# Performance work log

Measured on AMD Instinct MI355X. Metric: run time of the kernel, lower is better.

The kernel has to match this reference:

```python
import jax, jax.numpy as jnp
import numpy as np

BN_EPS = 1e-3  # keras BatchNormalization default epsilon
D = 128
EDGE_DIM = 16
N_NODES = 50000
N_EDGES = 800000

def setup_inputs() -> dict:
    key = jax.random.key(0)
    ks = jax.random.split(key, 12)
    inp = {
        'node_feat': jax.random.normal(ks[0], (N_NODES, D), jnp.float32),
        'edge_feat': jax.random.normal(ks[1], (N_EDGES, EDGE_DIM), jnp.float32),
        'src': jax.random.randint(ks[2], (N_EDGES,), 0, N_NODES, jnp.int32),
        'dst': jax.random.randint(ks[3], (N_EDGES,), 0, N_NODES, jnp.int32),
        # EdgeEncoder: Dense(2*D) -> Dense(D)
        'We1': jax.random.normal(ks[4], (EDGE_DIM, 2 * D), jnp.float32) * 0.05,
        'be1': jnp.zeros((2 * D,), jnp.float32),
        'We2': jax.random.normal(ks[5], (2 * D, D), jnp.float32) * 0.05,
        'be2': jnp.zeros((D,), jnp.float32),
        # GINNodeUpdate eps (shape (1,) weight)
        'eps': jax.random.normal(ks[6], (1,), jnp.float32) * 0.05,
        # MLP: Dense(2*D) -> BN -> relu -> Dense(D)
        'Wm1': jax.random.normal(ks[7], (D, 2 * D), jnp.float32) * 0.05,
        'bm1': jnp.zeros((2 * D,), jnp.float32),
        'g1': jnp.ones((2 * D,), jnp.float32),
        'b1': jnp.zeros((2 * D,), jnp.float32),
        'm1': jnp.zeros((2 * D,), jnp.float32),
        'v1': jnp.ones((2 * D,), jnp.float32),
        'Wm2': jax.random.normal(ks[8], (2 * D, D), jnp.float32) * 0.05,
        'bm2': jnp.zeros((D,), jnp.float32),
        # outer BN after MLP
        'g2': jnp.ones((D,), jnp.float32),
        'b2': jnp.zeros((D,), jnp.float32),
        'm2': jnp.zeros((D,), jnp.float32),
        'v2': jnp.ones((D,), jnp.float32),
    }
    return inp

def _bn(x, gamma, beta, mean, var):
    return (x - mean) * jax.lax.rsqrt(var + BN_EPS) * gamma + beta

def reference(node_feat, edge_feat, src, dst, We1, be1, We2, be2, eps,
              Wm1, bm1, g1, b1, m1, v1, Wm2, bm2, g2, b2, m2, v2):
    # EdgeEncoder on raw edge features -> [E, D]
    e = (edge_feat @ We1 + be1) @ We2 + be2
    # combine_type='sum' with broadcast-from-sender gather, message_fn=relu
    msg = jax.nn.relu(e + node_feat[src])          # [E, D]
    # pool_to_receiver: segment-sum scatter to target nodes
    pooled = jax.ops.segment_sum(msg, dst, num_segments=node_feat.shape[0])  # [N, D]
    # GINNodeUpdate: MLP((1+eps)*node + pooled) then BN
    h = (1.0 + eps) * node_feat + pooled
    h = jax.nn.relu(_bn(h @ Wm1 + bm1, g1, b1, m1, v1)) @ Wm2 + bm2
    return _bn(h, g2, b2, m2, v2)
```

## Files before the change

kernel.cpp:

```cpp
#include <hip/hip_runtime.h>

#define D 128
#define TWO_D 256
#define EDIM 16
#define BN_EPS 1e-3f
#define NT 16
#define CAP 48

__device__ __forceinline__ float4 fma4(float4 a, float s, float4 w) {
    a.x = fmaf(s, w.x, a.x);
    a.y = fmaf(s, w.y, a.y);
    a.z = fmaf(s, w.z, a.z);
    a.w = fmaf(s, w.w, a.w);
    return a;
}

__device__ __forceinline__ unsigned bf16pk(float a, float b) {
    unsigned ua = __float_as_uint(a); ua = (ua + 0x7FFFu + ((ua >> 16) & 1u)) >> 16;
    unsigned ub = __float_as_uint(b); ub = (ub + 0x7FFFu + ((ub >> 16) & 1u)) & 0xFFFF0000u;
    return ua | ub;
}
__device__ __forceinline__ float bf_lo(unsigned u) { return __uint_as_float(u << 16); }
__device__ __forceinline__ float bf_hi(unsigned u) { return __uint_as_float(u & 0xFFFF0000u); }

__device__ __forceinline__ void mlp_tile(
    int tid, int n0, const float* hbuf, float* tbuf,
    const float* __restrict__ Wm1, const float* __restrict__ bm1,
    const float* __restrict__ g1, const float* __restrict__ b1,
    const float* __restrict__ m1, const float* __restrict__ v1,
    const float* __restrict__ Wm2, const float* __restrict__ bm2,
    const float* __restrict__ g2, const float* __restrict__ b2,
    const float* __restrict__ m2, const float* __restrict__ v2,
    float* __restrict__ out)
{
    {
        const int g = tid >> 7;
        const int c = tid & 127;
        float acc[8][2];
#pragma unroll
        for (int n = 0; n < 8; ++n) { acc[n][0] = 0.f; acc[n][1] = 0.f; }

        for (int k0 = 0; k0 < D; k0 += 4) {
            float wa[4], wb[4];
#pragma unroll
            for (int kk = 0; kk < 4; ++kk) {
                wa[kk] = Wm1[(k0 + kk) * TWO_D + c];
                wb[kk] = Wm1[(k0 + kk) * TWO_D + c + 128];
            }
#pragma unroll
            for (int n = 0; n < 8; ++n) {
                float4 h4 = *(const float4*)&hbuf[(g * 8 + n) * D + k0];
                acc[n][0] = fmaf(h4.x, wa[0], acc[n][0]);
                acc[n][0] = fmaf(h4.y, wa[1], acc[n][0]);
                acc[n][0] = fmaf(h4.z, wa[2], acc[n][0]);
                acc[n][0] = fmaf(h4.w, wa[3], acc[n][0]);
                acc[n][1] = fmaf(h4.x, wb[0], acc[n][1]);
                acc[n][1] = fmaf(h4.y, wb[1], acc[n][1]);
                acc[n][1] = fmaf(h4.z, wb[2], acc[n][1]);
                acc[n][1] = fmaf(h4.w, wb[3], acc[n][1]);
            }
        }
        const float s1a = g1[c] * rsqrtf(v1[c] + BN_EPS);
        const float t1a = (bm1[c] - m1[c]) * s1a + b1[c];
        const int c2 = c + 128;
        const float s1b = g1[c2] * rsqrtf(v1[c2] + BN_EPS);
        const float t1b = (bm1[c2] - m1[c2]) * s1b + b1[c2];
#pragma unroll
        for (int n = 0; n < 8; ++n) {
            tbuf[(g * 8 + n) * TWO_D + c]  = fmaxf(fmaf(acc[n][0], s1a, t1a), 0.f);
            tbuf[(g * 8 + n) * TWO_D + c2] = fmaxf(fmaf(acc[n][1], s1b, t1b), 0.f);
        }
    }
    __syncthreads();

    {
        const int q = tid >> 6;
        const int d = tid & 63;
        float acc2[4][2];
#pragma unroll
        for (int n = 0; n < 4; ++n) { acc2[n][0] = 0.f; acc2[n][1] = 0.f; }

        for (int k0 = 0; k0 < TWO_D; k0 += 4) {
            float wa[4], wb[4];
#pragma unroll
            for (int kk = 0; kk < 4; ++kk) {
                wa[kk] = Wm2[(k0 + kk) * D + d];
                wb[kk] = Wm2[(k0 + kk) * D + d + 64];
            }
#pragma unroll
            for (int n = 0; n < 4; ++n) {
                float4 t4 = *(const float4*)&tbuf[(q * 4 + n) * TWO_D + k0];
                acc2[n][0] = fmaf(t4.x, wa[0], acc2[n][0]);
                acc2[n][0] = fmaf(t4.y, wa[1], acc2[n][0]);
                acc2[n][0] = fmaf(t4.z, wa[2], acc2[n][0]);
                acc2[n][0] = fmaf(t4.w, wa[3], acc2[n][0]);
                acc2[n][1] = fmaf(t4.x, wb[0], acc2[n][1]);
                acc2[n][1] = fmaf(t4.y, wb[1], acc2[n][1]);
                acc2[n][1] = fmaf(t4.z, wb[2], acc2[n][1]);
                acc2[n][1] = fmaf(t4.w, wb[3], acc2[n][1]);
            }
        }
        const float s2a = g2[d] * rsqrtf(v2[d] + BN_EPS);
        const float t2a = (bm2[d] - m2[d]) * s2a + b2[d];
        const int d2 = d + 64;
        const float s2b = g2[d2] * rsqrtf(v2[d2] + BN_EPS);
        const float t2b = (bm2[d2] - m2[d2]) * s2b + b2[d2];
#pragma unroll
        for (int n = 0; n < 4; ++n) {
            size_t row = (size_t)(n0 + q * 4 + n) * D;
            out[row + d]  = fmaf(acc2[n][0], s2a, t2a);
            out[row + d2] = fmaf(acc2[n][1], s2b, t2b);
        }
    }
}

__global__ __launch_bounds__(128)
void fold_and_zero(const float* __restrict__ We1,
                   const float* __restrict__ be1,
                   const float* __restrict__ We2,
                   const float* __restrict__ be2,
                   float* __restrict__ Wf,
                   float* __restrict__ bf,
                   int*   __restrict__ cnt,
                   int n_nodes)
{
    const int b = blockIdx.x;
    if (b <= EDIM) {
        const int k = b, d = threadIdx.x;
        if (k < EDIM) {
            float acc = 0.f;
            for (int j = 0; j < TWO_D; j += 4) {
                acc = fmaf(We1[k * TWO_D + j + 0], We2[(j + 0) * D + d], acc);
                acc = fmaf(We1[k * TWO_D + j + 1], We2[(j + 1) * D + d], acc);
                acc = fmaf(We1[k * TWO_D + j + 2], We2[(j + 2) * D + d], acc);
                acc = fmaf(We1[k * TWO_D + j + 3], We2[(j + 3) * D + d], acc);
            }
            Wf[k * D + d] = acc;
        } else {
            float acc = be2[d];
            for (int j = 0; j < TWO_D; j += 4) {
                acc = fmaf(be1[j + 0], We2[(j + 0) * D + d], acc);
                acc = fmaf(be1[j + 1], We2[(j + 1) * D + d], acc);
                acc = fmaf(be1[j + 2], We2[(j + 2) * D + d], acc);
                acc = fmaf(be1[j + 3], We2[(j + 3) * D + d], acc);
            }
            bf[d] = acc;
        }
    } else {
        int i = (b - (EDIM + 1)) * 128 + threadIdx.x;
        if (i < n_nodes) cnt[i] = 0;
    }
}

__global__ __launch_bounds__(256)
void scatter_ef(const float* __restrict__ edge_feat,
                const int* __restrict__ src, const int* __restrict__ dst,
                int* __restrict__ cnt,
                int* __restrict__ s_src,
                uint4* __restrict__ s_ef,
                int n_edges)
{
    int i = blockIdx.x * blockDim.x + threadIdx.x;
    if (i >= n_edges) return;
    const int d = dst[i];
    const float4* e4 = (const float4*)(edge_feat + (size_t)i * EDIM);
    const float4 f0 = e4[0], f1 = e4[1], f2 = e4[2], f3 = e4[3];
    const int s = src[i];
    const int pos = atomicAdd(&cnt[d], 1);
    if (pos < CAP) {
        const size_t r = (size_t)d * CAP + pos;
        s_src[r] = s;
        s_ef[r * 2 + 0] = make_uint4(bf16pk(f0.x, f0.y), bf16pk(f0.z, f0.w),
                                     bf16pk(f1.x, f1.y), bf16pk(f1.z, f1.w));
        s_ef[r * 2 + 1] = make_uint4(bf16pk(f2.x, f2.y), bf16pk(f2.z, f2.w),
                                     bf16pk(f3.x, f3.y), bf16pk(f3.z, f3.w));
    }
}

__global__ __launch_bounds__(256, 3)
void fused_ef(const uint4* __restrict__ s_ef,
              const int*   __restrict__ s_src,
              const int*   __restrict__ cnt,
              const float* __restrict__ node_feat,
              const float* __restrict__ Wf,
              const float* __restrict__ bf,
              const float* __restrict__ eps,
              const float* __restrict__ Wm1, const float* __restrict__ bm1,
              const float* __restrict__ g1, const float* __restrict__ b1,
              const float* __restrict__ m1, const float* __restrict__ v1,
              const float* __restrict__ Wm2, const float* __restrict__ bm2,
              const float* __restrict__ g2, const float* __restrict__ b2,
              const float* __restrict__ m2, const float* __restrict__ v2,
              float* __restrict__ out)
{
    __shared__ float hbuf[NT * D];
    __shared__ float tbuf[NT * TWO_D];

    const int tid = threadIdx.x;
    const int n0  = blockIdx.x * NT;
    const float ep = 1.0f + eps[0];

    {
        const int wv   = tid >> 6;
        const int lane = tid & 63;
        const int sub  = lane >> 5;
        const int q    = lane & 31;

        const float4* Wf4 = (const float4*)Wf;
        float4 wf[EDIM];
#pragma unroll
        for (int k = 0; k < EDIM; ++k) wf[k] = Wf4[k * 32 + q];
        const float4 bf4 = ((const float4*)bf)[q];

        for (int i = 0; i < 4; ++i) {
            const int node = n0 + wv * 4 + i;
            const int mt = min(cnt[node], CAP);
            float4 acc = {0.f, 0.f, 0.f, 0.f};

            if (mt > 0) {
                const size_t rbase = (size_t)node * CAP;
                const int srcl = s_src[rbase + min(lane, mt - 1)];

                int e = min(sub, mt - 1);
                uint4 cpa = s_ef[(rbase + e) * 2 + 0];
                uint4 cpb = s_ef[(rbase + e) * 2 + 1];
                int cs = __shfl(srcl, e);
                float4 cnf = *(const float4*)(node_feat + (size_t)cs * D + q * 4);

                const int jmax = (mt + 1) >> 1;
                for (int j = 0; j < jmax; ++j) {
                    uint4 npa = cpa, npb = cpb;
                    float4 nnf = cnf;
                    if (j + 1 < jmax) {
                        const int e2 = min(2 * (j + 1) + sub, mt - 1);
                        npa = s_ef[(rbase + e2) * 2 + 0];
                        npb = s_ef[(rbase + e2) * 2 + 1];
                        const int ns = __shfl(srcl, e2);
                        nnf = *(const float4*)(node_feat + (size_t)ns * D + q * 4);
                    }
                    float4 a = bf4;
                    a = fma4(a, bf_lo(cpa.x), wf[0]);  a = fma4(a, bf_hi(cpa.x), wf[1]);
                    a = fma4(a, bf_lo(cpa.y), wf[2]);  a = fma4(a, bf_hi(cpa.y), wf[3]);
                    a = fma4(a, bf_lo(cpa.z), wf[4]);  a = fma4(a, bf_hi(cpa.z), wf[5]);
                    a = fma4(a, bf_lo(cpa.w), wf[6]);  a = fma4(a, bf_hi(cpa.w), wf[7]);
                    a = fma4(a, bf_lo(cpb.x), wf[8]);  a = fma4(a, bf_hi(cpb.x), wf[9]);
                    a = fma4(a, bf_lo(cpb.y), wf[10]); a = fma4(a, bf_hi(cpb.y), wf[11]);
                    a = fma4(a, bf_lo(cpb.z), wf[12]); a = fma4(a, bf_hi(cpb.z), wf[13]);
                    a = fma4(a, bf_lo(cpb.w), wf[14]); a = fma4(a, bf_hi(cpb.w), wf[15]);
                    a.x = fmaxf(a.x + cnf.x, 0.f);
                    a.y = fmaxf(a.y + cnf.y, 0.f);
                    a.z = fmaxf(a.z + cnf.z, 0.f);
                    a.w = fmaxf(a.w + cnf.w, 0.f);
                    if (2 * j + sub < mt) {
                        acc.x += a.x; acc.y += a.y; acc.z += a.z; acc.w += a.w;
                    }
                    cpa = npa; cpb = npb; cnf = nnf;
                }
            }
            acc.x += __shfl_xor(acc.x, 32);
            acc.y += __shfl_xor(acc.y, 32);
            acc.z += __shfl_xor(acc.z, 32);
            acc.w += __shfl_xor(acc.w, 32);

            if (sub == 0) {
                const float4 nfo = *(const float4*)(node_feat + (size_t)node * D + q * 4);
                float4 hv;
                hv.x = fmaf(ep, nfo.x, acc.x);
                hv.y = fmaf(ep, nfo.y, acc.y);
                hv.z = fmaf(ep, nfo.z, acc.z);
                hv.w = fmaf(ep, nfo.w, acc.w);
                *(float4*)&hbuf[(wv * 4 + i) * D + q * 4] = hv;
            }
        }
    }
    __syncthreads();

    mlp_tile(tid, n0, hbuf, tbuf, Wm1, bm1, g1, b1, m1, v1,
             Wm2, bm2, g2, b2, m2, v2, out);
}

__global__ __launch_bounds__(256)
void hist_kernel(const int* __restrict__ dst, int* __restrict__ counts, int n_edges)
{
    int i = blockIdx.x * blockDim.x + threadIdx.x;
    if (i < n_edges) atomicAdd(&counts[dst[i]], 1);
}

__global__ __launch_bounds__(1024)
void scan_kernel(const int* __restrict__ counts,
                 int* __restrict__ row_ptr, int* __restrict__ cursor, int n)
{
    __shared__ int part[1024];
    const int t = threadIdx.x;
    const int chunk = (n + 1023) / 1024;
    const int lo = t * chunk;
    const int hi = min(lo + chunk, n);
    int s = 0;
    for (int i = lo; i < hi; ++i) s += counts[i];
    part[t] = s;
    __syncthreads();
    for (int off = 1; off < 1024; off <<= 1) {
        int v = (t >= off) ? part[t - off] : 0;
        __syncthreads();
        part[t] += v;
        __syncthreads();
    }
    int base = (t > 0) ? part[t - 1] : 0;
    for (int i = lo; i < hi; ++i) {
        row_ptr[i] = base;
        cursor[i]  = base;
        base += counts[i];
    }
    if (t == 1023) row_ptr[n] = part[1023];
}

__global__ __launch_bounds__(256)
void scatter_csr(const int* __restrict__ src, const int* __restrict__ dst,
                 int* __restrict__ cursor, int2* __restrict__ s_se, int n_edges)
{
    int i = blockIdx.x * blockDim.x + threadIdx.x;
    if (i < n_edges) {
        int d = dst[i];
        int pos = atomicAdd(&cursor[d], 1);
        s_se[pos] = make_int2(src[i], i);
    }
}

__global__ __launch_bounds__(256, 3)
void fused_csr(const float* __restrict__ edge_feat,
               const int2*  __restrict__ s_se,
               const int*   __restrict__ row_ptr,
               const float* __restrict__ node_feat,
               const float* __restrict__ Wf, const float* __restrict__ bf,
               const float* __restrict__ eps,
               const float* __restrict__ Wm1, const float* __restrict__ bm1,
               const float* __restrict__ g1, const float* __restrict__ b1,
               const float* __restrict__ m1, const float* __restrict__ v1,
               const float* __restrict__ Wm2, const float* __restrict__ bm2,
               const float* __restrict__ g2, const float* __restrict__ b2,
               const float* __restrict__ m2, const float* __restrict__ v2,
               float* __restrict__ out)
{
    __shared__ float hbuf[NT * D];
    __shared__ float tbuf[NT * TWO_D];

    const int tid = threadIdx.x;
    const int n0  = blockIdx.x * NT;
    const float ep = 1.0f + eps[0];

    {
        const int wv   = tid >> 6;
        const int lane = tid & 63;
        const int sub  = lane >> 5;
        const int q    = lane & 31;

        const float4* Wf4 = (const float4*)Wf;
        float4 wf[EDIM];
#pragma unroll
        for (int k = 0; k < EDIM; ++k) wf[k] = Wf4[k * 32 + q];
        const float4 bf4 = ((const float4*)bf)[q];

        for (int i = 0; i < 4; ++i) {
            const int node = n0 + wv * 4 + i;
            const int lo = row_ptr[node];
            const int mt = row_ptr[node + 1] - lo;
            float4 acc = {0.f, 0.f, 0.f, 0.f};

            for (int base = 0; base < mt; base += 64) {
                const int m = min(mt - base, 64);
                const int2 se_l = s_se[lo + base + min(lane, m - 1)];
                const int jmax = (m + 1) >> 1;

                int sx = __shfl(se_l.x, sub);
                int sy = __shfl(se_l.y, sub);
                const float4* e4 = (const float4*)(edge_feat + (size_t)sy * EDIM);
                float4 cf0 = e4[0], cf1 = e4[1], cf2 = e4[2], cf3 = e4[3];
                float4 cnf = *(const float4*)(node_feat + (size_t)sx * D + q * 4);

                for (int j = 0; j < jmax; ++j) {
                    float4 pf0 = cf0, pf1 = cf1, pf2 = cf2, pf3 = cf3, pnf = cnf;
                    if (j + 1 < jmax) {
                        const int idx2 = 2 * (j + 1) + sub;
                        int sx2 = __shfl(se_l.x, idx2);
                        int sy2 = __shfl(se_l.y, idx2);
                        const float4* n4 = (const float4*)(edge_feat + (size_t)sy2 * EDIM);
                        pf0 = n4[0]; pf1 = n4[1]; pf2 = n4[2]; pf3 = n4[3];
                        pnf = *(const float4*)(node_feat + (size_t)sx2 * D + q * 4);
                    }
                    float4 a = bf4;
                    a = fma4(a, cf0.x, wf[0]);  a = fma4(a, cf0.y, wf[1]);
                    a = fma4(a, cf0.z, wf[2]);  a = fma4(a, cf0.w, wf[3]);
                    a = fma4(a, cf1.x, wf[4]);  a = fma4(a, cf1.y, wf[5]);
                    a = fma4(a, cf1.z, wf[6]);  a = fma4(a, cf1.w, wf[7]);
                    a = fma4(a, cf2.x, wf[8]);  a = fma4(a, cf2.y, wf[9]);
                    a = fma4(a, cf2.z, wf[10]); a = fma4(a, cf2.w, wf[11]);
                    a = fma4(a, cf3.x, wf[12]); a = fma4(a, cf3.y, wf[13]);
                    a = fma4(a, cf3.z, wf[14]); a = fma4(a, cf3.w, wf[15]);
                    a.x = fmaxf(a.x + cnf.x, 0.f);
                    a.y = fmaxf(a.y + cnf.y, 0.f);
                    a.z = fmaxf(a.z + cnf.z, 0.f);
                    a.w = fmaxf(a.w + cnf.w, 0.f);
                    if (2 * j + sub < m) {
                        acc.x += a.x; acc.y += a.y; acc.z += a.z; acc.w += a.w;
                    }
                    cf0 = pf0; cf1 = pf1; cf2 = pf2; cf3 = pf3; cnf = pnf;
                }
            }
            acc.x += __shfl_xor(acc.x, 32);
            acc.y += __shfl_xor(acc.y, 32);
            acc.z += __shfl_xor(acc.z, 32);
            acc.w += __shfl_xor(acc.w, 32);

            if (sub == 0) {
                const float4 nfo = *(const float4*)(node_feat + (size_t)node * D + q * 4);
                float4 hv;
                hv.x = fmaf(ep, nfo.x, acc.x);
                hv.y = fmaf(ep, nfo.y, acc.y);
                hv.z = fmaf(ep, nfo.z, acc.z);
                hv.w = fmaf(ep, nfo.w, acc.w);
                *(float4*)&hbuf[(wv * 4 + i) * D + q * 4] = hv;
            }
        }
    }
    __syncthreads();

    mlp_tile(tid, n0, hbuf, tbuf, Wm1, bm1, g1, b1, m1, v1,
             Wm2, bm2, g2, b2, m2, v2, out);
}

extern "C" void kernel_launch(void* const* d_in, const int* in_sizes, int n_in,
                              void* d_out, int out_size, void* d_ws, size_t ws_size,
                              hipStream_t stream) {
    const float* node_feat = (const float*)d_in[0];
    const float* edge_feat = (const float*)d_in[1];
    const int*   src       = (const int*)d_in[2];
    const int*   dst       = (const int*)d_in[3];
    const float* We1       = (const float*)d_in[4];
    const float* be1       = (const float*)d_in[5];
    const float* We2       = (const float*)d_in[6];
    const float* be2       = (const float*)d_in[7];
    const float* eps       = (const float*)d_in[8];
    const float* Wm1       = (const float*)d_in[9];
    const float* bm1       = (const float*)d_in[10];
    const float* g1        = (const float*)d_in[11];
    const float* b1        = (const float*)d_in[12];
    const float* m1        = (const float*)d_in[13];
    const float* v1        = (const float*)d_in[14];
    const float* Wm2       = (const float*)d_in[15];
    const float* bm2       = (const float*)d_in[16];
    const float* g2        = (const float*)d_in[17];
    const float* b2        = (const float*)d_in[18];
    const float* m2        = (const float*)d_in[19];
    const float* v2        = (const float*)d_in[20];

    const int n_nodes = in_sizes[0] / D;
    const int n_edges = in_sizes[2];
    float* out = (float*)d_out;

    char* wsc = (char*)d_ws;
    size_t off = 0;
    float* Wf = (float*)(wsc + off); off += (size_t)EDIM * D * 4;
    float* bf = (float*)(wsc + off); off += (size_t)D * 4;
    int* cnt  = (int*)(wsc + off);   off += (size_t)n_nodes * 4;
    off = (off + 15) & ~(size_t)15;
    int* s_srcp = (int*)(wsc + off); off += (size_t)n_nodes * CAP * 4;
    off = (off + 15) & ~(size_t)15;
    uint4* s_efp = (uint4*)(wsc + off); off += (size_t)n_nodes * CAP * 32;
    const size_t primary_need = off;

    if (ws_size >= primary_need) {
        fold_and_zero<<<EDIM + 1 + (n_nodes + 127) / 128, 128, 0, stream>>>(
            We1, be1, We2, be2, Wf, bf, cnt, n_nodes);

        scatter_ef<<<(n_edges + 255) / 256, 256, 0, stream>>>(
            edge_feat, src, dst, cnt, s_srcp, s_efp, n_edges);

        fused_ef<<<n_nodes / NT, 256, 0, stream>>>(
            s_efp, s_srcp, cnt, node_feat, Wf, bf, eps,
            Wm1, bm1, g1, b1, m1, v1, Wm2, bm2, g2, b2, m2, v2, out);
    } else {
        int* counts  = cnt;
        int* row_ptr = counts + n_nodes;
        int* cursor  = row_ptr + n_nodes + 1;
        size_t ofs = (size_t)((char*)(cursor + n_nodes) - wsc);
        ofs = (ofs + 7) & ~(size_t)7;
        int2* s_se = (int2*)(wsc + ofs);

        fold_and_zero<<<EDIM + 1 + (n_nodes + 127) / 128, 128, 0, stream>>>(
            We1, be1, We2, be2, Wf, bf, counts, n_nodes);
        hist_kernel<<<(n_edges + 255) / 256, 256, 0, stream>>>(dst, counts, n_edges);
        scan_kernel<<<1, 1024, 0, stream>>>(counts, row_ptr, cursor, n_nodes);
        scatter_csr<<<(n_edges + 255) / 256, 256, 0, stream>>>(
            src, dst, cursor, s_se, n_edges);

        fused_csr<<<n_nodes / NT, 256, 0, stream>>>(
            edge_feat, s_se, row_ptr, node_feat, Wf, bf, eps,
            Wm1, bm1, g1, b1, m1, v1, Wm2, bm2, g2, b2, m2, v2, out);
    }
}
```

Measured before the change: 404.3 us.

## Run fused node MLP in packed fp16 with dot2 accumulation

Stores the aggregated node features and hidden activations in shared memory as packed fp16 pairs and computes both MLP matmuls with the packed fp16 dot2 instruction, accumulating in fp32. Weights are read as fp32 and converted to fp16 pairs inside the loop, and the output column mapping is reorganised so each thread handles two adjacent columns. The goal is to halve shared-memory traffic and FMA count in the MLP stage. In exchange it adds conversion work and loses precision (fp16 range and rounding) on activations and weights.

```diff
diff --git a/kernel.cpp b/kernel.cpp
--- a/kernel.cpp
+++ b/kernel.cpp
@@ -7,6 +7,8 @@
 #define NT 16
 #define CAP 48
 
+typedef _Float16 h2_t __attribute__((ext_vector_type(2)));
+
 __device__ __forceinline__ float4 fma4(float4 a, float s, float4 w) {
     a.x = fmaf(s, w.x, a.x);
     a.y = fmaf(s, w.y, a.y);
@@ -22,6 +24,22 @@
 }
 __device__ __forceinline__ float bf_lo(unsigned u) { return __uint_as_float(u << 16); }
 __device__ __forceinline__ float bf_hi(unsigned u) { return __uint_as_float(u & 0xFFFF0000u); }
+
+__device__ __forceinline__ unsigned pk2(float a, float b) {
+    h2_t h; h.x = (_Float16)a; h.y = (_Float16)b;
+    unsigned u; __builtin_memcpy(&u, &h, 4); return u;
+}
+__device__ __forceinline__ h2_t uph(unsigned u) {
+    h2_t h; __builtin_memcpy(&h, &u, 4); return h;
+}
+__device__ __forceinline__ float fdot2h(unsigned a, unsigned b, float c) {
+#if __has_builtin(__builtin_amdgcn_fdot2)
+    return __builtin_amdgcn_fdot2(uph(a), uph(b), c, false);
+#else
+    h2_t ha = uph(a), hb = uph(b);
+    return c + (float)ha.x * (float)hb.x + (float)ha.y * (float)hb.y;
+#endif
+}
 
 __device__ __forceinline__ void mlp_tile(
     int tid, int n0, const float* hbuf, float* tbuf,
@@ -178,13 +196,13 @@
 }
 
 __global__ __launch_bounds__(256, 3)
-void fused_ef(const uint4* __restrict__ s_ef,
-              const int*   __restrict__ s_src,
-              const int*   __restrict__ cnt,
-              const float* __restrict__ node_feat,
-              const float* __restrict__ Wf,
-              const float* __restrict__ bf,
-              const float* __restrict__ eps,
+void fused_ef(const uint4*   __restrict__ s_ef,
+              const int*     __restrict__ s_src,
+              const int*     __restrict__ cnt,
+              const float*   __restrict__ node_feat,
+              const float*   __restrict__ Wf,
+              const float*   __restrict__ bf,
+              const float*   __restrict__ eps,
               const float* __restrict__ Wm1, const float* __restrict__ bm1,
               const float* __restrict__ g1, const float* __restrict__ b1,
               const float* __restrict__ m1, const float* __restrict__ v1,
@@ -193,8 +211,8 @@
               const float* __restrict__ m2, const float* __restrict__ v2,
               float* __restrict__ out)
 {
-    __shared__ float hbuf[NT * D];
-    __shared__ float tbuf[NT * TWO_D];
+    __shared__ unsigned hbuf[NT * 64];
+    __shared__ unsigned tbuf[NT * 128];
 
     const int tid = threadIdx.x;
     const int n0  = blockIdx.x * NT;
@@ -264,19 +282,113 @@
 
             if (sub == 0) {
                 const float4 nfo = *(const float4*)(node_feat + (size_t)node * D + q * 4);
-                float4 hv;
-                hv.x = fmaf(ep, nfo.x, acc.x);
-                hv.y = fmaf(ep, nfo.y, acc.y);
-                hv.z = fmaf(ep, nfo.z, acc.z);
-                hv.w = fmaf(ep, nfo.w, acc.w);
-                *(float4*)&hbuf[(wv * 4 + i) * D + q * 4] = hv;
+                float hx = fmaf(ep, nfo.x, acc.x);
+                float hy = fmaf(ep, nfo.y, acc.y);
+                float hz = fmaf(ep, nfo.z, acc.z);
+                float hw = fmaf(ep, nfo.w, acc.w);
+                uint2 hv = make_uint2(pk2(hx, hy), pk2(hz, hw));
+                *(uint2*)&hbuf[(wv * 4 + i) * 64 + 2 * q] = hv;
             }
         }
     }
     __syncthreads();
 
-    mlp_tile(tid, n0, hbuf, tbuf, Wm1, bm1, g1, b1, m1, v1,
-             Wm2, bm2, g2, b2, m2, v2, out);
+    {
+        const int g = tid >> 7;
+        const int c = tid & 127;
+        float acc[8][2];
+#pragma unroll
+        for (int n = 0; n < 8; ++n) { acc[n][0] = 0.f; acc[n][1] = 0.f; }
+
+        for (int kp0 = 0; kp0 < 64; kp0 += 4) {
+            unsigned wpa[4], wpb[4];
+#pragma unroll
+            for (int j = 0; j < 4; ++j) {
+                const int k0 = 2 * (kp0 + j);
+                const float2 lo = *(const float2*)&Wm1[(size_t)k0 * TWO_D + 2 * c];
+                const float2 hi = *(const float2*)&Wm1[(size_t)(k0 + 1) * TWO_D + 2 * c];
+                wpa[j] = pk2(lo.x, hi.x);
+                wpb[j] = pk2(lo.y, hi.y);
+            }
+#pragma unroll
+            for (int n = 0; n < 8; ++n) {
+                uint4 h4 = *(const uint4*)&hbuf[(g * 8 + n) * 64 + kp0];
+                acc[n][0] = fdot2h(h4.x, wpa[0], acc[n][0]);
+                acc[n][1] = fdot2h(h4.x, wpb[0], acc[n][1]);
+                acc[n][0] = fdot2h(h4.y, wpa[1], acc[n][0]);
+                acc[n][1] = fdot2h(h4.y, wpb[1], acc[n][1]);
+                acc[n][0] = fdot2h(h4.z, wpa[2], acc[n][0]);
+                acc[n][1] = fdot2h(h4.z, wpb[2], acc[n][1]);
+                acc[n][0] = fdot2h(h4.w, wpa[3], acc[n][0]);
+                acc[n][1] = fdot2h(h4.w, wpb[3], acc[n][1]);
+            }
+        }
+        const float2 gg = *(const float2*)&g1[2 * c];
+        const float2 vv = *(const float2*)&v1[2 * c];
+        const float2 bb = *(const float2*)&b1[2 * c];
+        const float2 mm = *(const float2*)&m1[2 * c];
+        const float2 bm = *(const float2*)&bm1[2 * c];
+        const float s1a = gg.x * rsqrtf(vv.x + BN_EPS);
+        const float t1a = (bm.x - mm.x) * s1a + bb.x;
+        const float s1b = gg.y * rsqrtf(vv.y + BN_EPS);
+        const float t1b = (bm.y - mm.y) * s1b + bb.y;
+#pragma unroll
+        for (int n = 0; n < 8; ++n) {
+            float ta = fmaxf(fmaf(acc[n][0], s1a, t1a), 0.f);
+            float tb = fmaxf(fmaf(acc[n][1], s1b, t1b), 0.f);
+            tbuf[(g * 8 + n) * 128 + c] = pk2(ta, tb);
+        }
+    }
+    __syncthreads();
+
+    {
+        const int qq = tid >> 6;
+        const int dd = tid & 63;
+        float acc2[4][2];
+#pragma unroll
+        for (int n = 0; n < 4; ++n) { acc2[n][0] = 0.f; acc2[n][1] = 0.f; }
+
+        for (int kp0 = 0; kp0 < 128; kp0 += 4) {
+            unsigned wpa[4], wpb[4];
+#pragma unroll
+            for (int j = 0; j < 4; ++j) {
+                const int k0 = 2 * (kp0 + j);
+                const float2 lo = *(const float2*)&Wm2[(size_t)k0 * D + 2 * dd];
+                const float2 hi = *(const float2*)&Wm2[(size_t)(k0 + 1) * D + 2 * dd];
+                wpa[j] = pk2(lo.x, hi.x);
+                wpb[j] = pk2(lo.y, hi.y);
+            }
+#pragma unroll
+            for (int n = 0; n < 4; ++n) {
+                uint4 t4 = *(const uint4*)&tbuf[(qq * 4 + n) * 128 + kp0];
+                acc2[n][0] = fdot2h(t4.x, wpa[0], acc2[n][0]);
+                acc2[n][1] = fdot2h(t4.x, wpb[0], acc2[n][1]);
+                acc2[n][0] = fdot2h(t4.y, wpa[1], acc2[n][0]);
+                acc2[n][1] = fdot2h(t4.y, wpb[1], acc2[n][1]);
+                acc2[n][0] = fdot2h(t4.z, wpa[2], acc2[n][0]);
+                acc2[n][1] = fdot2h(t4.z, wpb[2], acc2[n][1]);
+                acc2[n][0] = fdot2h(t4.w, wpa[3], acc2[n][0]);
+                acc2[n][1] = fdot2h(t4.w, wpb[3], acc2[n][1]);
+            }
+        }
+        const float2 gg = *(const float2*)&g2[2 * dd];
+        const float2 vv = *(const float2*)&v2[2 * dd];
+        const float2 bb = *(const float2*)&b2[2 * dd];
+        const float2 mm = *(const float2*)&m2[2 * dd];
+        const float2 bm = *(const float2*)&bm2[2 * dd];
+        const float s2a = gg.x * rsqrtf(vv.x + BN_EPS);
+        const float t2a = (bm.x - mm.x) * s2a + bb.x;
+        const float s2b = gg.y * rsqrtf(vv.y + BN_EPS);
+        const float t2b = (bm.y - mm.y) * s2b + bb.y;
+#pragma unroll
+        for (int n = 0; n < 4; ++n) {
+            size_t row = (size_t)(n0 + qq * 4 + n) * D;
+            float2 o;
+            o.x = fmaf(acc2[n][0], s2a, t2a);
+            o.y = fmaf(acc2[n][1], s2b, t2b);
+            *(float2*)&out[row + 2 * dd] = o;
+        }
+    }
 }
 
 __global__ __launch_bounds__(256)
```

New measurement: 446.2 us. +10.4%, slower.

## Run node-update MLP on fp16 MFMA instead of scalar FMA tile

Applied to the files above, without the earlier changes.

Replaces the scalar fp32 mlp_tile in fused_ef with two fp16 MFMA 16x16x32 GEMM stages. The aggregated node features and hidden activations are stored in shared memory as packed fp16 with padded strides to avoid bank conflicts. Weights are loaded from global memory and converted to fp16 on every block, and the batch-norm affine transforms are folded into the MFMA epilogues. This targets the per-block cost of the dense MLP at the price of reduced precision and strided scalar weight loads.

```diff
diff --git a/kernel.cpp b/kernel.cpp
--- a/kernel.cpp
+++ b/kernel.cpp
@@ -6,6 +6,12 @@
 #define BN_EPS 1e-3f
 #define NT 16
 #define CAP 48
+#define HS 68
+#define TS 132
+
+typedef _Float16 h2_t __attribute__((ext_vector_type(2)));
+typedef _Float16 half8 __attribute__((ext_vector_type(8)));
+typedef float floatx4 __attribute__((ext_vector_type(4)));
 
 __device__ __forceinline__ float4 fma4(float4 a, float s, float4 w) {
     a.x = fmaf(s, w.x, a.x);
@@ -22,6 +28,11 @@
 }
 __device__ __forceinline__ float bf_lo(unsigned u) { return __uint_as_float(u << 16); }
 __device__ __forceinline__ float bf_hi(unsigned u) { return __uint_as_float(u & 0xFFFF0000u); }
+
+__device__ __forceinline__ unsigned pk2(float a, float b) {
+    h2_t h; h.x = (_Float16)a; h.y = (_Float16)b;
+    unsigned u; __builtin_memcpy(&u, &h, 4); return u;
+}
 
 __device__ __forceinline__ void mlp_tile(
     int tid, int n0, const float* hbuf, float* tbuf,
@@ -178,13 +189,13 @@
 }
 
 __global__ __launch_bounds__(256, 3)
-void fused_ef(const uint4* __restrict__ s_ef,
-              const int*   __restrict__ s_src,
-              const int*   __restrict__ cnt,
-              const float* __restrict__ node_feat,
-              const float* __restrict__ Wf,
-              const float* __restrict__ bf,
-              const float* __restrict__ eps,
+void fused_ef(const uint4*   __restrict__ s_ef,
+              const int*     __restrict__ s_src,
+              const int*     __restrict__ cnt,
+              const float*   __restrict__ node_feat,
+              const float*   __restrict__ Wf,
+              const float*   __restrict__ bf,
+              const float*   __restrict__ eps,
               const float* __restrict__ Wm1, const float* __restrict__ bm1,
               const float* __restrict__ g1, const float* __restrict__ b1,
               const float* __restrict__ m1, const float* __restrict__ v1,
@@ -193,8 +204,8 @@
               const float* __restrict__ m2, const float* __restrict__ v2,
               float* __restrict__ out)
 {
-    __shared__ float hbuf[NT * D];
-    __shared__ float tbuf[NT * TWO_D];
+    __shared__ unsigned hbuf[NT * HS];
+    __shared__ unsigned tbuf[NT * TS];
 
     const int tid = threadIdx.x;
     const int n0  = blockIdx.x * NT;
@@ -264,19 +275,92 @@
 
             if (sub == 0) {
                 const float4 nfo = *(const float4*)(node_feat + (size_t)node * D + q * 4);
-                float4 hv;
-                hv.x = fmaf(ep, nfo.x, acc.x);
-                hv.y = fmaf(ep, nfo.y, acc.y);
-                hv.z = fmaf(ep, nfo.z, acc.z);
-                hv.w = fmaf(ep, nfo.w, acc.w);
-                *(float4*)&hbuf[(wv * 4 + i) * D + q * 4] = hv;
+                float hx = fmaf(ep, nfo.x, acc.x);
+                float hy = fmaf(ep, nfo.y, acc.y);
+                float hz = fmaf(ep, nfo.z, acc.z);
+                float hw = fmaf(ep, nfo.w, acc.w);
+                uint2 hv = make_uint2(pk2(hx, hy), pk2(hz, hw));
+                *(uint2*)&hbuf[(wv * 4 + i) * HS + 2 * q] = hv;
             }
         }
     }
     __syncthreads();
 
-    mlp_tile(tid, n0, hbuf, tbuf, Wm1, bm1, g1, b1, m1, v1,
-             Wm2, bm2, g2, b2, m2, v2, out);
+    const int w    = tid >> 6;
+    const int lane = tid & 63;
+    const int n15  = lane & 15;
+    const int q8   = lane >> 4;
+
+    {
+        half8 afr[4];
+#pragma unroll
+        for (int ks = 0; ks < 4; ++ks) {
+            uint4 u = *(const uint4*)&hbuf[n15 * HS + ks * 16 + q8 * 4];
+            __builtin_memcpy(&afr[ks], &u, 16);
+        }
+        floatx4 acc1[4];
+#pragma unroll
+        for (int t = 0; t < 4; ++t) acc1[t] = (floatx4){0.f, 0.f, 0.f, 0.f};
+
+#pragma unroll
+        for (int t = 0; t < 4; ++t) {
+            const int col = w * 64 + t * 16 + n15;
+#pragma unroll
+            for (int ks = 0; ks < 4; ++ks) {
+                const float* wp = &Wm1[(size_t)(ks * 32 + q8 * 8) * TWO_D + col];
+                half8 bfr;
+#pragma unroll
+                for (int j = 0; j < 8; ++j) bfr[j] = (_Float16)wp[(size_t)j * TWO_D];
+                acc1[t] = __builtin_amdgcn_mfma_f32_16x16x32_f16(afr[ks], bfr, acc1[t], 0, 0, 0);
+            }
+        }
+        _Float16* tb16 = (_Float16*)tbuf;
+#pragma unroll
+        for (int t = 0; t < 4; ++t) {
+            const int c = w * 64 + t * 16 + n15;
+            const float s1 = g1[c] * rsqrtf(v1[c] + BN_EPS);
+            const float t1 = (bm1[c] - m1[c]) * s1 + b1[c];
+#pragma unroll
+            for (int r = 0; r < 4; ++r) {
+                const int row = q8 * 4 + r;
+                tb16[row * (2 * TS) + c] = (_Float16)fmaxf(fmaf(acc1[t][r], s1, t1), 0.f);
+            }
+        }
+    }
+    __syncthreads();
+
+    {
+        floatx4 acc2[2];
+        acc2[0] = (floatx4){0.f, 0.f, 0.f, 0.f};
+        acc2[1] = (floatx4){0.f, 0.f, 0.f, 0.f};
+
+#pragma unroll
+        for (int ks = 0; ks < 8; ++ks) {
+            uint4 u = *(const uint4*)&tbuf[n15 * TS + ks * 16 + q8 * 4];
+            half8 afr;
+            __builtin_memcpy(&afr, &u, 16);
+#pragma unroll
+            for (int t = 0; t < 2; ++t) {
+                const int col = w * 32 + t * 16 + n15;
+                const float* wp = &Wm2[(size_t)(ks * 32 + q8 * 8) * D + col];
+                half8 bfr;
+#pragma unroll
+                for (int j = 0; j < 8; ++j) bfr[j] = (_Float16)wp[(size_t)j * D];
+                acc2[t] = __builtin_amdgcn_mfma_f32_16x16x32_f16(afr, bfr, acc2[t], 0, 0, 0);
+            }
+        }
+#pragma unroll
+        for (int t = 0; t < 2; ++t) {
+            const int c = w * 32 + t * 16 + n15;
+            const float s2 = g2[c] * rsqrtf(v2[c] + BN_EPS);
+            const float t2 = (bm2[c] - m2[c]) * s2 + b2[c];
+#pragma unroll
+            for (int r = 0; r < 4; ++r) {
+                const int row = q8 * 4 + r;
+                out[(size_t)(n0 + row) * D + c] = fmaf(acc2[t][r], s2, t2);
+            }
+        }
+    }
 }
 
 __global__ __launch_bounds__(256)
```

Result: faster. 335.8 us (-17.0%).
